# Kernel tuning notes

Hardware: AMD Instinct MI355X
Metric: run time of the kernel (lower is better)

Reference implementation:

```python
import jax, jax.numpy as jnp
import numpy as np
import math

B, S, D, H = 2, 2048, 1024, 16
DK = D // H  # 64
THETA = 500000.0


def setup_inputs() -> dict:
    key = jax.random.key(0)
    ks = jax.random.split(key, 6)
    x = jax.random.normal(ks[0], (B, S, D), dtype=jnp.float32)
    # RoPE frequencies: inv_freq = theta^{-(2i/dk)}, angles = pos * inv_freq
    inv_freq = 1.0 / (THETA ** (jnp.arange(0, DK, 2, dtype=jnp.float32) / DK))  # [DK/2]
    angles = jnp.arange(S, dtype=jnp.float32)[:, None] * inv_freq[None, :]      # [S, DK/2]
    freqs_cos = jnp.cos(angles)
    freqs_sin = jnp.sin(angles)
    # causal additive mask [B, S, S]: 0 on/below diagonal, -1e9 above
    causal = jnp.tril(jnp.ones((S, S), dtype=bool))
    mask = jnp.where(causal, 0.0, -1e9).astype(jnp.float32)
    mask = jnp.broadcast_to(mask, (B, S, S))
    scale = 0.02
    wq = jax.random.normal(ks[1], (D, D), dtype=jnp.float32) * scale
    wk = jax.random.normal(ks[2], (D, D), dtype=jnp.float32) * scale
    wv = jax.random.normal(ks[3], (D, D), dtype=jnp.float32) * scale
    wo = jax.random.normal(ks[4], (D, D), dtype=jnp.float32) * scale
    return {"x": x, "freqs_cos": freqs_cos, "freqs_sin": freqs_sin,
            "mask": mask, "wq": wq, "wk": wk, "wv": wv, "wo": wo}


def _apply_rope(t, cos, sin):
    # t: [B, S, H, DK]; cos/sin: [S, DK/2]
    tr = t.reshape(*t.shape[:-1], DK // 2, 2)
    t0, t1 = tr[..., 0], tr[..., 1]
    c = cos[None, :, None, :]
    s = sin[None, :, None, :]
    out = jnp.stack([t0 * c - t1 * s, t0 * s + t1 * c], axis=-1)
    return out.reshape(*t.shape)


def reference(x, freqs_cos, freqs_sin, mask, wq, wk, wv, wo):
    b, s, d = x.shape
    # nn.Linear(bias=False): y = x @ W^T, W is [out, in]
    q = jnp.einsum('bsd,ed->bse', x, wq).reshape(b, s, H, DK)
    k = jnp.einsum('bsd,ed->bse', x, wk).reshape(b, s, H, DK)
    v = jnp.einsum('bsd,ed->bse', x, wv).reshape(b, s, H, DK)
    q = _apply_rope(q, freqs_cos, freqs_sin)
    k = _apply_rope(k, freqs_cos, freqs_sin)
    inv_sqrt_dk = 1.0 / math.sqrt(DK)
    # scores: [B, H, S, S]
    scores = jnp.einsum('bqhd,bkhd->bhqk', q, k) * inv_sqrt_dk
    scores = scores + mask[:, None, :, :]
    # NOTE: the original module divides by sqrt(d_k) a SECOND time before softmax
    attn = jax.nn.softmax(scores * inv_sqrt_dk, axis=-1)
    out = jnp.einsum('bhqk,bkhd->bqhd', attn, v).reshape(b, s, d)
    return jnp.einsum('bsd,ed->bse', out, wo)
```

## Files before the change

kernel.cpp:

```cpp
#include <hip/hip_runtime.h>
#include <stdint.h>

#define Bq 2
#define Sq 2048
#define Dq 1024
#define Hq 16
#define DKq 64

typedef unsigned short u16;
typedef __attribute__((ext_vector_type(8))) __bf16 bf8;
typedef __attribute__((ext_vector_type(4))) __bf16 bf4;
typedef __attribute__((ext_vector_type(4))) float fx4;
typedef __attribute__((ext_vector_type(8))) unsigned short us8;
typedef __attribute__((ext_vector_type(4))) unsigned short us4;

__device__ __forceinline__ u16 f2bf(float f) {
    union { float f; unsigned int i; } v; v.f = f;
    unsigned int r = v.i + 0x7FFFu + ((v.i >> 16) & 1u);
    return (u16)(r >> 16);
}

__device__ __forceinline__ void gll16(const void* g, void* l) {
    typedef __attribute__((address_space(1))) void GV;
    typedef __attribute__((address_space(3))) void LV;
    __builtin_amdgcn_global_load_lds((GV*)g, (LV*)l, 16, 0, 0);
}

template<int N> __device__ __forceinline__ void waitv() {
    asm volatile("s_waitcnt vmcnt(%0)" :: "n"(N) : "memory");
}
__device__ __forceinline__ void SB() { __builtin_amdgcn_sched_barrier(0); }

__global__ void __launch_bounds__(256) cvt_all(const float* __restrict__ x,
                                               const float* __restrict__ wq,
                                               const float* __restrict__ wk,
                                               const float* __restrict__ wv,
                                               const float* __restrict__ wo,
                                               u16* __restrict__ ws) {
    int blk = blockIdx.x;
    const float* s;
    u16* d;
    int i;
    if (blk < 4096)      { s = x;  d = ws;           i = blk * 256 + threadIdx.x; }
    else if (blk < 5120) { s = wq; d = ws + 4194304; i = (blk - 4096) * 256 + threadIdx.x; }
    else if (blk < 6144) { s = wk; d = ws + 5242880; i = (blk - 5120) * 256 + threadIdx.x; }
    else if (blk < 7168) { s = wv; d = ws + 6291456; i = (blk - 6144) * 256 + threadIdx.x; }
    else                 { s = wo; d = ws + 7340032; i = (blk - 7168) * 256 + threadIdx.x; }
    float4 v = *(const float4*)(s + (size_t)i * 4);
    us4 o;
    o[0] = f2bf(v.x); o[1] = f2bf(v.y); o[2] = f2bf(v.z); o[3] = f2bf(v.w);
    *(us4*)(d + (size_t)i * 4) = o;
}

template<int MODE>
__global__ void __launch_bounds__(512, 4) gemm_bt(
    const u16* __restrict__ A,
    const u16* __restrict__ W0, const u16* __restrict__ W1, const u16* __restrict__ W2,
    u16* __restrict__ O0, u16* __restrict__ O1, u16* __restrict__ O2,
    float* __restrict__ Of,
    const float* __restrict__ fc, const float* __restrict__ fs)
{
    constexpr int K = 1024;
    constexpr int NT = 32;
    constexpr int BM = MODE ? 128 : 64;
    constexpr int BN = MODE ? 256 : 128;
    constexpr int WM = BM / 2;
    constexpr int WN = BN / 4;
    constexpr int MI = WM / 16;
    constexpr int NJ = WN / 16;
    constexpr int BOPS = BN / 128;
    constexpr int ASZ = BM * 32;
    constexpr int BSZ = BN * 32;
    __shared__ __align__(16) u16 As[3 * ASZ];
    __shared__ __align__(16) u16 Bs[3 * BSZ];
    const int tid = threadIdx.x;
    const int lane = tid & 63, wid = tid >> 6;
    const int wr = wid >> 2, wc = wid & 3;
    const int fr = lane & 15, fq = lane >> 4;

    int wgid = blockIdx.x;
    int Xc = wgid & 7, jj = wgid >> 3;
    int by, bx, bz;
    if (MODE == 1) {
        int T = Xc * 48 + jj;
        by = T / 12;
        int p = T - by * 12;
        bz = p >> 2; bx = p & 3;
    } else {
        int T = Xc * 64 + jj;
        by = T >> 3; bx = T & 7; bz = 0;
    }
    const int m0 = by * BM, n0 = bx * BN;

    const u16* Wm = W0;
    u16* Ob = O0;
    if (MODE == 1) {
        if (bz == 1)      { Wm = W1; Ob = O1; }
        else if (bz == 2) { Wm = W2; Ob = O2; }
    }

    const int arow = tid >> 2;
    const int sw = ((tid & 3) ^ (arow & 3)) * 8;
    const u16* ga = A  + (size_t)(m0 + arow) * K + sw;
    const u16* gb = Wm + (size_t)(n0 + arow) * K + sw;

    fx4 acc[MI][NJ] = {};

    auto STAGE = [&](int t, int b) {
        if (MODE == 1) {
            gll16(ga + t * 32, As + b * ASZ + tid * 8);
            #pragma unroll
            for (int c = 0; c < BOPS; ++c)
                gll16(gb + (size_t)c * 128 * K + t * 32, Bs + b * BSZ + c * 4096 + tid * 8);
        } else {
            if (tid < 256) gll16(ga + t * 32, As + b * ASZ + tid * 8);
            gll16(gb + t * 32, Bs + b * BSZ + tid * 8);
        }
    };
    auto WAITP = [&]() {
        if (MODE == 1) { waitv<6>(); }
        else { if (wid < 4) { waitv<4>(); } else { waitv<2>(); } }
    };
    auto WAITL = [&]() {
        if (MODE == 1) { waitv<3>(); }
        else { if (wid < 4) { waitv<2>(); } else { waitv<1>(); } }
    };

    const int kq = (fq ^ (fr & 3)) * 8;

    STAGE(0, 0); STAGE(1, 1); STAGE(2, 2);
    WAITP();
    SB(); __builtin_amdgcn_s_barrier(); SB();

    #pragma unroll 1
    for (int t = 0; t < NT; ++t) {
        const u16* Ab = As + (t % 3) * ASZ;
        const u16* Bb = Bs + (t % 3) * BSZ;
        bf8 af[MI], bfv[NJ];
        #pragma unroll
        for (int mi = 0; mi < MI; ++mi)
            af[mi] = *(const bf8*)(&Ab[(wr * WM + mi * 16 + fr) * 32 + kq]);
        #pragma unroll
        for (int nj = 0; nj < NJ; ++nj)
            bfv[nj] = *(const bf8*)(&Bb[(wc * WN + nj * 16 + fr) * 32 + kq]);
        if (t + 2 < NT) STAGE(t + 2, (t + 2) % 3);
        __builtin_amdgcn_s_setprio(1);
        #pragma unroll
        for (int mi = 0; mi < MI; ++mi)
            #pragma unroll
            for (int nj = 0; nj < NJ; ++nj)
                acc[mi][nj] = __builtin_amdgcn_mfma_f32_16x16x32_bf16(af[mi], bfv[nj], acc[mi][nj], 0, 0, 0);
        __builtin_amdgcn_s_setprio(0);
        SB();
        if (t < NT - 2)       { WAITL(); }
        else if (t == NT - 2) { waitv<0>(); }
        SB(); __builtin_amdgcn_s_barrier(); SB();
    }

    if (MODE == 0) {
        #pragma unroll
        for (int mi = 0; mi < MI; ++mi)
            #pragma unroll
            for (int nj = 0; nj < NJ; ++nj)
                #pragma unroll
                for (int r = 0; r < 4; ++r) {
                    int m = m0 + wr * WM + mi * 16 + fq * 4 + r;
                    int n = n0 + wc * WN + nj * 16 + fr;
                    Of[(size_t)m * 1024 + n] = acc[mi][nj][r];
                }
    } else if (bz == 2) {
        #pragma unroll
        for (int mi = 0; mi < MI; ++mi)
            #pragma unroll
            for (int nj = 0; nj < NJ; ++nj) {
                int n = n0 + wc * WN + nj * 16 + fr;
                int mb = m0 + wr * WM + mi * 16 + fq * 4;
                int b = mb >> 11, s = mb & 2047;
                int h = n >> 6, dk = n & 63;
                bf4 pk;
                #pragma unroll
                for (int r = 0; r < 4; ++r) pk[r] = (__bf16)acc[mi][nj][r];
                *(bf4*)((__bf16*)Ob + (((size_t)(b * Hq + h)) * DKq + dk) * Sq + s) = pk;
            }
    } else {
        #pragma unroll
        for (int mi = 0; mi < MI; ++mi)
            #pragma unroll
            for (int nj = 0; nj < NJ; ++nj) {
                int n = n0 + wc * WN + nj * 16 + fr;
                int h = n >> 6, dk = n & 63;
                int ip = dk >> 1;
                float sgn = (dk & 1) ? 1.f : -1.f;
                #pragma unroll
                for (int r = 0; r < 4; ++r) {
                    int m = m0 + wr * WM + mi * 16 + fq * 4 + r;
                    int b = m >> 11, s = m & 2047;
                    float v = acc[mi][nj][r];
                    float pv = __shfl_xor(v, 1);
                    float c  = fc[s * 32 + ip];
                    float sn = fs[s * 32 + ip];
                    float o = v * c + sgn * pv * sn;
                    ((__bf16*)Ob)[(((size_t)(b * Hq + h)) * Sq + s) * DKq + dk] = (__bf16)o;
                }
            }
    }
}

__device__ __forceinline__ int swz(int row) { return ((row & 7) ^ ((row >> 3) & 7)) << 4; }

__global__ void __launch_bounds__(512, 4) attn_k(const u16* __restrict__ Q,
                                                 const u16* __restrict__ Kg,
                                                 const u16* __restrict__ Vtg,
                                                 u16* __restrict__ AO) {
    int L = blockIdx.x + 32 * blockIdx.y;
    int X = L & 7, C = L >> 3;
    const int bh = X * 4 + (C & 3);
    const int Qt = 31 - (C >> 2);
    const int b = bh >> 4, h = bh & 15;
    const int tid = threadIdx.x, lane = tid & 63, wid = tid >> 6;
    const int wq4 = wid & 3, par = wid >> 2;
    const int fr = lane & 15, fq = lane >> 4;
    const int swzfr = swz(fr);

    __shared__ __align__(16) u16 Ks[2][64 * 64];
    __shared__ __align__(16) u16 Vs[2][64 * 64];
    __shared__ __align__(16) u16 Ps[8][16 * 64];
    __shared__ float Lx[4][64];

    const u16* Kp = Kg  + (size_t)bh * Sq * 64;
    const u16* Vp = Vtg + (size_t)bh * 64 * Sq;
    const int q0 = Qt * 64;
    const int nt = Qt + 1;
    const int NS = (nt + 1) >> 1;

    bf8 qf0, qf1;
    {
        const u16* Qp = Q + ((size_t)bh * Sq + q0) * 64;
        int qr = wq4 * 16 + fr;
        qf0 = *(const bf8*)(Qp + qr * 64 + fq * 8);
        qf1 = *(const bf8*)(Qp + qr * 64 + fq * 8 + 32);
    }

    fx4 oacc[4] = {};
    float l_loc = 0.f;

    const int srow = tid >> 3;
    const int sce  = (tid & 7) * 8;
    const int ldst = srow * 128 + (((tid & 7) * 16) ^ swz(srow));

    us8 kreg[2], vreg[2];
    #pragma unroll
    for (int c = 0; c < 2; ++c) {
        int t = c < nt ? c : nt - 1;
        kreg[c] = *(const us8*)(Kp + ((size_t)t * 64 + srow) * 64 + sce);
        vreg[c] = *(const us8*)(Vp + (size_t)srow * Sq + t * 64 + sce);
    }
    #pragma unroll
    for (int c = 0; c < 2; ++c) {
        *(us8*)((char*)Ks[c] + ldst) = kreg[c];
        *(us8*)((char*)Vs[c] + ldst) = vreg[c];
    }
    if (NS > 1) {
        #pragma unroll
        for (int c = 0; c < 2; ++c) {
            int t = 2 + c < nt ? 2 + c : nt - 1;
            kreg[c] = *(const us8*)(Kp + ((size_t)t * 64 + srow) * 64 + sce);
            vreg[c] = *(const us8*)(Vp + (size_t)srow * Sq + t * 64 + sce);
        }
    }
    __syncthreads();

    #pragma unroll 1
    for (int sp = 0; sp < NS; ++sp) {
        const int t = 2 * sp + par;
        if (t < nt) {
            const char* Kb = (const char*)Ks[par];
            const char* Vb = (const char*)Vs[par];
            char* Pw = (char*)Ps[wid] + fr * 128;

            fx4 sf[4];
            __builtin_amdgcn_s_setprio(1);
            #pragma unroll
            for (int sj = 0; sj < 4; ++sj) {
                int krow = sj * 16 + fr;
                bf8 kf0 = *(const bf8*)(Kb + krow * 128 + ((fq * 16) ^ swz(krow)));
                bf8 kf1 = *(const bf8*)(Kb + krow * 128 + ((64 + fq * 16) ^ swz(krow)));
                fx4 a = {0.f, 0.f, 0.f, 0.f};
                a = __builtin_amdgcn_mfma_f32_16x16x32_bf16(kf0, qf0, a, 0, 0, 0);
                a = __builtin_amdgcn_mfma_f32_16x16x32_bf16(kf1, qf1, a, 0, 0, 0);
                sf[sj] = a;
            }
            __builtin_amdgcn_s_setprio(0);

            float pv[4][4];
            #pragma unroll
            for (int sj = 0; sj < 4; ++sj)
                #pragma unroll
                for (int r = 0; r < 4; ++r)
                    pv[sj][r] = __expf(sf[sj][r] * 0.015625f);
            if (t == Qt) {
                int ql = wq4 * 16 + fr;
                #pragma unroll
                for (int sj = 0; sj < 4; ++sj)
                    #pragma unroll
                    for (int r = 0; r < 4; ++r)
                        if (sj * 16 + fq * 4 + r > ql) pv[sj][r] = 0.f;
            }
            #pragma unroll
            for (int sj = 0; sj < 4; ++sj) {
                bf4 w;
                #pragma unroll
                for (int r = 0; r < 4; ++r) { w[r] = (__bf16)pv[sj][r]; l_loc += pv[sj][r]; }
                *(bf4*)(Pw + ((sj * 32 + fq * 8) ^ swzfr)) = w;
            }

            __builtin_amdgcn_s_setprio(1);
            #pragma unroll
            for (int kk = 0; kk < 2; ++kk) {
                bf8 pf = *(const bf8*)(Pw + ((kk * 64 + fq * 16) ^ swzfr));
                #pragma unroll
                for (int mf = 0; mf < 4; ++mf) {
                    int vrow = mf * 16 + fr;
                    bf8 vf = *(const bf8*)(Vb + vrow * 128 + ((kk * 64 + fq * 16) ^ swz(vrow)));
                    oacc[mf] = __builtin_amdgcn_mfma_f32_16x16x32_bf16(vf, pf, oacc[mf], 0, 0, 0);
                }
            }
            __builtin_amdgcn_s_setprio(0);
        }
        __syncthreads();
        if (sp + 1 < NS) {
            #pragma unroll
            for (int c = 0; c < 2; ++c) {
                *(us8*)((char*)Ks[c] + ldst) = kreg[c];
                *(us8*)((char*)Vs[c] + ldst) = vreg[c];
            }
            if (sp + 2 < NS) {
                #pragma unroll
                for (int c = 0; c < 2; ++c) {
                    int tt = 2 * (sp + 2) + c; if (tt > nt - 1) tt = nt - 1;
                    kreg[c] = *(const us8*)(Kp + ((size_t)tt * 64 + srow) * 64 + sce);
                    vreg[c] = *(const us8*)(Vp + (size_t)srow * Sq + tt * 64 + sce);
                }
            }
            __syncthreads();
        }
    }

    l_loc += __shfl_xor(l_loc, 16);
    l_loc += __shfl_xor(l_loc, 32);
    if (par == 1) {
        float* ob = (float*)Ps + wq4 * 1024;
        #pragma unroll
        for (int mf = 0; mf < 4; ++mf)
            *(fx4*)(ob + lane * 16 + mf * 4) = oacc[mf];
        Lx[wq4][lane] = l_loc;
    }
    __syncthreads();
    if (par == 0) {
        const float* ob = (float*)Ps + wq4 * 1024;
        float lt = l_loc + Lx[wq4][lane];
        float linv = __builtin_amdgcn_rcpf(lt);
        int s = q0 + wq4 * 16 + fr;
        #pragma unroll
        for (int mf = 0; mf < 4; ++mf) {
            fx4 oh = *(const fx4*)(ob + lane * 16 + mf * 4);
            bf4 pk;
            #pragma unroll
            for (int r = 0; r < 4; ++r) pk[r] = (__bf16)((oacc[mf][r] + oh[r]) * linv);
            *(bf4*)((__bf16*)AO + ((size_t)(b * Sq + s)) * Dq + h * 64 + mf * 16 + fq * 4) = pk;
        }
    }
}

extern "C" void kernel_launch(void* const* d_in, const int* in_sizes, int n_in,
                              void* d_out, int out_size, void* d_ws, size_t ws_size,
                              hipStream_t stream) {
    const float* x  = (const float*)d_in[0];
    const float* fc = (const float*)d_in[1];
    const float* fs = (const float*)d_in[2];
    const float* wq = (const float*)d_in[4];
    const float* wk = (const float*)d_in[5];
    const float* wv = (const float*)d_in[6];
    const float* wo = (const float*)d_in[7];
    float* out = (float*)d_out;

    u16* ws  = (u16*)d_ws;
    u16* xb  = ws;
    u16* wqb = ws + 4194304;
    u16* wkb = ws + 5242880;
    u16* wvb = ws + 6291456;
    u16* wob = ws + 7340032;
    u16* Qb  = ws + 8388608;
    u16* Kb  = ws + 12582912;
    u16* Vb  = ws + 16777216;
    u16* AOb = ws + 20971520;

    cvt_all<<<8192, 256, 0, stream>>>(x, wq, wk, wv, wo, ws);

    gemm_bt<1><<<384, 512, 0, stream>>>(xb, wqb, wkb, wvb, Qb, Kb, Vb, nullptr, fc, fs);

    dim3 g2(32, 32, 1);
    attn_k<<<g2, 512, 0, stream>>>(Qb, Kb, Vb, AOb);

    gemm_bt<0><<<512, 512, 0, stream>>>(AOb, wob, nullptr, nullptr,
                                        nullptr, nullptr, nullptr, out, nullptr, nullptr);
}
```

Measured before the change: 104.2 us.

## Load K/V fragments directly from global into registers, drop LDS staging and split-KV waves

The attention kernel no longer stages K and V tiles through shared memory with block barriers. Each of four waves per block now loads its own MFMA operand fragments for K and V straight from global memory into registers, double-buffering K across iterations. The two-way split over KV tiles, and the cross-wave reduction it needed, are removed, so each wave walks every tile for its 16 query rows. This removes LDS traffic and __syncthreads, but every wave now refetches K/V from global/L2 rather than sharing it, uses more registers (launch bounds become 256 threads, 3 blocks), and halves the parallelism within a block.

```diff
diff --git a/kernel.cpp b/kernel.cpp
--- a/kernel.cpp
+++ b/kernel.cpp
@@ -8,6 +8,7 @@
 #define DKq 64
 
 typedef unsigned short u16;
+typedef unsigned int u32;
 typedef __attribute__((ext_vector_type(8))) __bf16 bf8;
 typedef __attribute__((ext_vector_type(4))) __bf16 bf4;
 typedef __attribute__((ext_vector_type(4))) float fx4;
@@ -208,167 +209,124 @@
 
 __device__ __forceinline__ int swz(int row) { return ((row & 7) ^ ((row >> 3) & 7)) << 4; }
 
-__global__ void __launch_bounds__(512, 4) attn_k(const u16* __restrict__ Q,
+__global__ void __launch_bounds__(256, 3) attn_k(const u16* __restrict__ Q,
                                                  const u16* __restrict__ Kg,
                                                  const u16* __restrict__ Vtg,
                                                  u16* __restrict__ AO) {
-    int L = blockIdx.x + 32 * blockIdx.y;
+    int L = blockIdx.x;
     int X = L & 7, C = L >> 3;
     const int bh = X * 4 + (C & 3);
     const int Qt = 31 - (C >> 2);
     const int b = bh >> 4, h = bh & 15;
     const int tid = threadIdx.x, lane = tid & 63, wid = tid >> 6;
-    const int wq4 = wid & 3, par = wid >> 2;
     const int fr = lane & 15, fq = lane >> 4;
     const int swzfr = swz(fr);
 
-    __shared__ __align__(16) u16 Ks[2][64 * 64];
-    __shared__ __align__(16) u16 Vs[2][64 * 64];
-    __shared__ __align__(16) u16 Ps[8][16 * 64];
-    __shared__ float Lx[4][64];
-
-    const u16* Kp = Kg  + (size_t)bh * Sq * 64;
-    const u16* Vp = Vtg + (size_t)bh * 64 * Sq;
+    __shared__ __align__(16) u16 Ps[4][16 * 64];
+
+    const u16* Kp = Kg  + (size_t)bh * Sq * 64 + fr * 64 + fq * 8;
+    const u16* Vp = Vtg + ((size_t)bh * 64 + fr) * Sq + fq * 8;
     const int q0 = Qt * 64;
     const int nt = Qt + 1;
-    const int NS = (nt + 1) >> 1;
 
     bf8 qf0, qf1;
     {
-        const u16* Qp = Q + ((size_t)bh * Sq + q0) * 64;
-        int qr = wq4 * 16 + fr;
-        qf0 = *(const bf8*)(Qp + qr * 64 + fq * 8);
-        qf1 = *(const bf8*)(Qp + qr * 64 + fq * 8 + 32);
+        const u16* Qp = Q + ((size_t)bh * Sq + q0 + wid * 16 + fr) * 64 + fq * 8;
+        qf0 = *(const bf8*)(Qp);
+        qf1 = *(const bf8*)(Qp + 32);
     }
 
     fx4 oacc[4] = {};
     float l_loc = 0.f;
-
-    const int srow = tid >> 3;
-    const int sce  = (tid & 7) * 8;
-    const int ldst = srow * 128 + (((tid & 7) * 16) ^ swz(srow));
-
-    us8 kreg[2], vreg[2];
-    #pragma unroll
-    for (int c = 0; c < 2; ++c) {
-        int t = c < nt ? c : nt - 1;
-        kreg[c] = *(const us8*)(Kp + ((size_t)t * 64 + srow) * 64 + sce);
-        vreg[c] = *(const us8*)(Vp + (size_t)srow * Sq + t * 64 + sce);
-    }
-    #pragma unroll
-    for (int c = 0; c < 2; ++c) {
-        *(us8*)((char*)Ks[c] + ldst) = kreg[c];
-        *(us8*)((char*)Vs[c] + ldst) = vreg[c];
-    }
-    if (NS > 1) {
-        #pragma unroll
-        for (int c = 0; c < 2; ++c) {
-            int t = 2 + c < nt ? 2 + c : nt - 1;
-            kreg[c] = *(const us8*)(Kp + ((size_t)t * 64 + srow) * 64 + sce);
-            vreg[c] = *(const us8*)(Vp + (size_t)srow * Sq + t * 64 + sce);
-        }
-    }
-    __syncthreads();
-
-    #pragma unroll 1
-    for (int sp = 0; sp < NS; ++sp) {
-        const int t = 2 * sp + par;
-        if (t < nt) {
-            const char* Kb = (const char*)Ks[par];
-            const char* Vb = (const char*)Vs[par];
-            char* Pw = (char*)Ps[wid] + fr * 128;
-
-            fx4 sf[4];
-            __builtin_amdgcn_s_setprio(1);
-            #pragma unroll
-            for (int sj = 0; sj < 4; ++sj) {
-                int krow = sj * 16 + fr;
-                bf8 kf0 = *(const bf8*)(Kb + krow * 128 + ((fq * 16) ^ swz(krow)));
-                bf8 kf1 = *(const bf8*)(Kb + krow * 128 + ((64 + fq * 16) ^ swz(krow)));
-                fx4 a = {0.f, 0.f, 0.f, 0.f};
-                a = __builtin_amdgcn_mfma_f32_16x16x32_bf16(kf0, qf0, a, 0, 0, 0);
-                a = __builtin_amdgcn_mfma_f32_16x16x32_bf16(kf1, qf1, a, 0, 0, 0);
-                sf[sj] = a;
-            }
-            __builtin_amdgcn_s_setprio(0);
-
-            float pv[4][4];
+    char* Pw = (char*)Ps[wid] + fr * 128;
+    const int ql = wid * 16 + fr;
+
+    bf8 kA[8], kB[8], vf[8];
+
+    auto LOADK = [&](bf8* kd, int t) {
+        #pragma unroll
+        for (int sj = 0; sj < 4; ++sj) {
+            const u16* p = Kp + (size_t)(t * 64 + sj * 16) * 64;
+            kd[2 * sj]     = *(const bf8*)(p);
+            kd[2 * sj + 1] = *(const bf8*)(p + 32);
+        }
+    };
+    auto LOADV = [&](int t) {
+        #pragma unroll
+        for (int mf = 0; mf < 4; ++mf) {
+            const u16* p = Vp + (size_t)(mf * 16) * Sq + t * 64;
+            vf[2 * mf]     = *(const bf8*)(p);
+            vf[2 * mf + 1] = *(const bf8*)(p + 32);
+        }
+    };
+
+    auto STEP = [&](const bf8* kf, int t) {
+        fx4 sf[4];
+        __builtin_amdgcn_s_setprio(1);
+        #pragma unroll
+        for (int sj = 0; sj < 4; ++sj) {
+            fx4 a = {0.f, 0.f, 0.f, 0.f};
+            a = __builtin_amdgcn_mfma_f32_16x16x32_bf16(kf[2 * sj],     qf0, a, 0, 0, 0);
+            a = __builtin_amdgcn_mfma_f32_16x16x32_bf16(kf[2 * sj + 1], qf1, a, 0, 0, 0);
+            sf[sj] = a;
+        }
+        __builtin_amdgcn_s_setprio(0);
+
+        float pv[4][4];
+        #pragma unroll
+        for (int sj = 0; sj < 4; ++sj)
+            #pragma unroll
+            for (int r = 0; r < 4; ++r)
+                pv[sj][r] = __expf(sf[sj][r] * 0.015625f);
+        if (t == Qt) {
             #pragma unroll
             for (int sj = 0; sj < 4; ++sj)
                 #pragma unroll
                 for (int r = 0; r < 4; ++r)
-                    pv[sj][r] = __expf(sf[sj][r] * 0.015625f);
-            if (t == Qt) {
-                int ql = wq4 * 16 + fr;
-                #pragma unroll
-                for (int sj = 0; sj < 4; ++sj)
-                    #pragma unroll
-                    for (int r = 0; r < 4; ++r)
-                        if (sj * 16 + fq * 4 + r > ql) pv[sj][r] = 0.f;
-            }
-            #pragma unroll
-            for (int sj = 0; sj < 4; ++sj) {
-                bf4 w;
-                #pragma unroll
-                for (int r = 0; r < 4; ++r) { w[r] = (__bf16)pv[sj][r]; l_loc += pv[sj][r]; }
-                *(bf4*)(Pw + ((sj * 32 + fq * 8) ^ swzfr)) = w;
-            }
-
+                    if (sj * 16 + fq * 4 + r > ql) pv[sj][r] = 0.f;
+        }
+        #pragma unroll
+        for (int sj = 0; sj < 4; ++sj) {
+            bf4 w;
+            #pragma unroll
+            for (int r = 0; r < 4; ++r) { w[r] = (__bf16)pv[sj][r]; l_loc += pv[sj][r]; }
+            *(bf4*)(Pw + ((sj * 32 + fq * 8) ^ swzfr)) = w;
+        }
+
+        #pragma unroll
+        for (int kk = 0; kk < 2; ++kk) {
+            bf8 pf = *(const bf8*)(Pw + ((kk * 64 + fq * 16) ^ swzfr));
             __builtin_amdgcn_s_setprio(1);
             #pragma unroll
-            for (int kk = 0; kk < 2; ++kk) {
-                bf8 pf = *(const bf8*)(Pw + ((kk * 64 + fq * 16) ^ swzfr));
-                #pragma unroll
-                for (int mf = 0; mf < 4; ++mf) {
-                    int vrow = mf * 16 + fr;
-                    bf8 vf = *(const bf8*)(Vb + vrow * 128 + ((kk * 64 + fq * 16) ^ swz(vrow)));
-                    oacc[mf] = __builtin_amdgcn_mfma_f32_16x16x32_bf16(vf, pf, oacc[mf], 0, 0, 0);
-                }
-            }
+            for (int mf = 0; mf < 4; ++mf)
+                oacc[mf] = __builtin_amdgcn_mfma_f32_16x16x32_bf16(vf[2 * mf + kk], pf, oacc[mf], 0, 0, 0);
             __builtin_amdgcn_s_setprio(0);
         }
-        __syncthreads();
-        if (sp + 1 < NS) {
-            #pragma unroll
-            for (int c = 0; c < 2; ++c) {
-                *(us8*)((char*)Ks[c] + ldst) = kreg[c];
-                *(us8*)((char*)Vs[c] + ldst) = vreg[c];
-            }
-            if (sp + 2 < NS) {
-                #pragma unroll
-                for (int c = 0; c < 2; ++c) {
-                    int tt = 2 * (sp + 2) + c; if (tt > nt - 1) tt = nt - 1;
-                    kreg[c] = *(const us8*)(Kp + ((size_t)tt * 64 + srow) * 64 + sce);
-                    vreg[c] = *(const us8*)(Vp + (size_t)srow * Sq + tt * 64 + sce);
-                }
-            }
-            __syncthreads();
+    };
+
+    LOADK(kA, 0);
+    #pragma unroll 1
+    for (int t = 0; t < nt; t += 2) {
+        LOADV(t);
+        if (t + 1 < nt) LOADK(kB, t + 1);
+        STEP(kA, t);
+        if (t + 1 < nt) {
+            LOADV(t + 1);
+            if (t + 2 < nt) LOADK(kA, t + 2);
+            STEP(kB, t + 1);
         }
     }
 
     l_loc += __shfl_xor(l_loc, 16);
     l_loc += __shfl_xor(l_loc, 32);
-    if (par == 1) {
-        float* ob = (float*)Ps + wq4 * 1024;
-        #pragma unroll
-        for (int mf = 0; mf < 4; ++mf)
-            *(fx4*)(ob + lane * 16 + mf * 4) = oacc[mf];
-        Lx[wq4][lane] = l_loc;
-    }
-    __syncthreads();
-    if (par == 0) {
-        const float* ob = (float*)Ps + wq4 * 1024;
-        float lt = l_loc + Lx[wq4][lane];
-        float linv = __builtin_amdgcn_rcpf(lt);
-        int s = q0 + wq4 * 16 + fr;
-        #pragma unroll
-        for (int mf = 0; mf < 4; ++mf) {
-            fx4 oh = *(const fx4*)(ob + lane * 16 + mf * 4);
-            bf4 pk;
-            #pragma unroll
-            for (int r = 0; r < 4; ++r) pk[r] = (__bf16)((oacc[mf][r] + oh[r]) * linv);
-            *(bf4*)((__bf16*)AO + ((size_t)(b * Sq + s)) * Dq + h * 64 + mf * 16 + fq * 4) = pk;
-        }
+    float linv = __builtin_amdgcn_rcpf(l_loc);
+    int s = q0 + wid * 16 + fr;
+    #pragma unroll
+    for (int mf = 0; mf < 4; ++mf) {
+        bf4 pk;
+        #pragma unroll
+        for (int r = 0; r < 4; ++r) pk[r] = (__bf16)(oacc[mf][r] * linv);
+        *(bf4*)((__bf16*)AO + ((size_t)(b * Sq + s)) * Dq + h * 64 + mf * 16 + fq * 4) = pk;
     }
 }
 
@@ -399,8 +357,7 @@
 
     gemm_bt<1><<<384, 512, 0, stream>>>(xb, wqb, wkb, wvb, Qb, Kb, Vb, nullptr, fc, fs);
 
-    dim3 g2(32, 32, 1);
-    attn_k<<<g2, 512, 0, stream>>>(Qb, Kb, Vb, AOb);
+    attn_k<<<1024, 256, 0, stream>>>(Qb, Kb, Vb, AOb);
 
     gemm_bt<0><<<512, 512, 0, stream>>>(AOb, wob, nullptr, nullptr,
                                         nullptr, nullptr, nullptr, out, nullptr, nullptr);
```

Result: slower. 193.5 us (+85.6%).
